# Kernel tuning notes

Hardware: AMD Instinct MI355X
Metric: run time of the kernel (lower is better)

Reference implementation:

```python
import jax, jax.numpy as jnp
import numpy as np

D_IN = 1024
D_OUT = 1024


def setup_inputs() -> dict:
    key = jax.random.key(0)
    kx, kq, kk, kv = jax.random.split(key, 4)
    B, T = 8, 2048
    x = jax.random.normal(kx, (B, T, D_IN), dtype=jnp.float32)
    # torch Linear weight is (d_out, d_in); we store transposed (d_in, d_out)
    s = 1.0 / np.sqrt(D_IN)
    Wq = jax.random.uniform(kq, (D_IN, D_OUT), jnp.float32, -s, s)
    Wk = jax.random.uniform(kk, (D_IN, D_OUT), jnp.float32, -s, s)
    Wv = jax.random.uniform(kv, (D_IN, D_OUT), jnp.float32, -s, s)
    return {"x": x, "Wq": Wq, "Wk": Wk, "Wv": Wv}


def reference(x, Wq, Wk, Wv):
    # x: (B, T, d_in)
    T = x.shape[1]
    d_out = Wq.shape[1]
    q = jnp.einsum('btd,de->bte', x, Wq)  # (B,T,d_out)
    k = jnp.einsum('btd,de->bte', x, Wk)
    v = jnp.einsum('btd,de->bte', x, Wv)
    scores = jnp.einsum('bqe,bke->bqk', q, k)  # (B,T,T)
    causal = jnp.tril(jnp.ones((T, T), dtype=bool))  # True = keep
    scores = jnp.where(causal[None], scores, -jnp.inf)
    weights = jax.nn.softmax(scores / jnp.sqrt(jnp.asarray(d_out, x.dtype)), axis=-1)
    # dropout p=0.0 -> identity
    return jnp.einsum('bqk,bke->bqe', weights, v)  # (B,T,d_out)
```

## Files before the change

### kernel.cpp

```cpp
#include <hip/hip_runtime.h>

using u16 = unsigned short;
typedef __bf16 bf16x8 __attribute__((ext_vector_type(8)));
typedef unsigned short u16x8 __attribute__((ext_vector_type(8)));
typedef float floatx4 __attribute__((ext_vector_type(4)));

__device__ __forceinline__ u16 f2bf(float f) {
  union { float f; unsigned u; } c; c.f = f;
  unsigned u = c.u;
  u += 0x7fffu + ((u >> 16) & 1u);
  return (u16)(u >> 16);
}
__device__ __forceinline__ float bf2f(u16 h) {
  union { unsigned u; float f; } c; c.u = ((unsigned)h) << 16; return c.f;
}

__device__ __forceinline__ void st_out(float* p, float v) { *p = v; }
__device__ __forceinline__ void st_out(u16* p, float v) { *p = f2bf(v); }

__device__ __forceinline__ void load16(const u16* g, u16* l) {
  __builtin_amdgcn_global_load_lds(
      (const __attribute__((address_space(1))) void*)g,
      (__attribute__((address_space(3))) void*)l, 16, 0, 0);
}

#define TILE 128
#define BK 64

template<typename OutT>
__device__ __forceinline__ void gemm_core(
    const u16* __restrict__ A, int lda, long sA,
    const u16* __restrict__ Bt, int ldb, long sB,
    OutT* __restrict__ C, int ldc, long sC,
    int kmax, int bx, int by, int bz, int tid)
{
  __shared__ u16 As[TILE * BK];
  __shared__ u16 Bs[TILE * BK];

  const u16* Ab = A + bz * sA + (long)by * TILE * lda;
  const u16* Bb = Bt + bz * sB + (long)bx * TILE * ldb;

  int lane = tid & 63;
  int wm = ((tid >> 7) & 1) * 64;
  int wn = ((tid >> 6) & 1) * 64;

  floatx4 acc[4][4] = {};
  int arow = wm + (lane & 15);
  int brow = wn + (lane & 15);
  int q = lane >> 4;

  for (int k0 = 0; k0 < kmax; k0 += BK) {
    __syncthreads();
#pragma unroll
    for (int h = 0; h < 4; h++) {
      int cc = tid + h * 256;
      int row = cc >> 3, gm = (cc & 7) ^ (row & 7);
      load16(Ab + (long)row * lda + k0 + gm * 8, &As[cc * 8]);
    }
#pragma unroll
    for (int h = 0; h < 4; h++) {
      int cc = tid + h * 256;
      int row = cc >> 3, gm = (cc & 7) ^ (row & 7);
      load16(Bb + (long)row * ldb + k0 + gm * 8, &Bs[cc * 8]);
    }
    __builtin_amdgcn_s_waitcnt(0);
    __syncthreads();

#pragma unroll
    for (int kp = 0; kp < 2; kp++) {
      bf16x8 a[4], b[4];
#pragma unroll
      for (int i = 0; i < 4; i++) {
        int r = arow + i * 16;
        a[i] = *(const bf16x8*)&As[(r * 8 + ((kp * 4 + q) ^ (r & 7))) * 8];
      }
#pragma unroll
      for (int j = 0; j < 4; j++) {
        int r = brow + j * 16;
        b[j] = *(const bf16x8*)&Bs[(r * 8 + ((kp * 4 + q) ^ (r & 7))) * 8];
      }
#pragma unroll
      for (int i = 0; i < 4; i++)
#pragma unroll
        for (int j = 0; j < 4; j++)
          acc[i][j] = __builtin_amdgcn_mfma_f32_16x16x32_bf16(a[i], b[j], acc[i][j], 0, 0, 0);
    }
  }

  OutT* Cb = C + bz * sC;
  int colbase = bx * TILE + wn + (lane & 15);
  int rowbase = by * TILE + wm + ((lane >> 4) << 2);
#pragma unroll
  for (int i = 0; i < 4; i++)
#pragma unroll
    for (int j = 0; j < 4; j++) {
      int col = colbase + j * 16;
#pragma unroll
      for (int r = 0; r < 4; r++)
        st_out(&Cb[(long)(rowbase + i * 16 + r) * ldc + col], acc[i][j][r]);
    }
}

template<typename OutT>
__global__ __launch_bounds__(256, 2)
void gemm_rect(const u16* __restrict__ A, int lda, long sA,
               const u16* __restrict__ Bt, int ldb, long sB,
               OutT* __restrict__ C, int ldc, long sC, int K,
               int l2gx, int nO8s)
{
  int L = blockIdx.x;
  int t = ((L & 7) << nO8s) | (L >> 3);
  int bx = t & ((1 << l2gx) - 1), by = t >> l2gx;
  gemm_core<OutT>(A, lda, sA, Bt, ldb, sB, C, ldc, sC, K, bx, by, blockIdx.y, threadIdx.x);
}

__global__ __launch_bounds__(256, 2)
void gemm_tri(const u16* __restrict__ A, int lda, long sA,
              const u16* __restrict__ Bt, int ldb, long sB,
              u16* __restrict__ C, int ldc, long sC, int K)
{
  int tp = blockIdx.x;
  int g = (tp & 7) * 17 + (tp >> 3);
  int sr = 0, sc = 0, pre = 0;
  for (;;) {
    int sz = (sr == sc) ? 3 : 4;
    if (pre + sz > g) break;
    pre += sz; ++sc;
    if (sc > sr) { ++sr; sc = 0; }
  }
  int w = g - pre;
  int r, c;
  if (sr == sc) { r = 2 * sr + (w > 0); c = 2 * sc + (w == 2); }
  else          { r = 2 * sr + (w >> 1); c = 2 * sc + (w & 1); }
  gemm_core<u16>(A, lda, sA, Bt, ldb, sB, C, ldc, sC, K, c, r, blockIdx.y, threadIdx.x);
}

__global__ __launch_bounds__(256, 2)
void gemm_opv(const u16* __restrict__ P, int lda, long sA,
              const u16* __restrict__ VT, int ldb, long sB,
              float* __restrict__ C, int ldc, long sC)
{
  int L = blockIdx.x;
  int j = L & 7, s = L >> 3;
  int by = (s < 8) ? 15 - j : j;
  int bx = s & 7;
  gemm_core<float>(P, lda, sA, VT, ldb, sB, C, ldc, sC,
                   (by + 1) * TILE, bx, by, blockIdx.y, threadIdx.x);
}

template<typename OutT>
__device__ __forceinline__ void gemm_core256(
    const u16* __restrict__ A, int lda, long sA,
    const u16* __restrict__ Bt, int ldb, long sB,
    OutT* __restrict__ C, int ldc, long sC,
    int kmax, int bx, int by, int bz, int tid, u16* lds)
{
  const u16* Ab = A + bz * sA + (long)by * 256 * lda;
  const u16* Bb = Bt + bz * sB + (long)bx * 256 * ldb;

  const int lane = tid & 63, wid = tid >> 6;
  const int wm = wid >> 2;
  const int wn = wid & 3;
  const int l15 = lane & 15, q = lane >> 4;

  const int cc0 = tid, cc1 = tid + 512;
  const int r0 = cc0 >> 3, g0 = (cc0 & 7) ^ (r0 & 7);
  const int r1 = cc1 >> 3, g1 = (cc1 & 7) ^ (r1 & 7);

  const int NK = kmax >> 6;

  floatx4 acc[8][4] = {};

  auto STAGE_A = [&](int k, int half, int buf) {
    const u16* g = Ab + (long)(half * 128) * lda + k * 64;
    load16(g + (long)r0 * lda + g0 * 8, lds + buf + half * 8192 + cc0 * 8);
    load16(g + (long)r1 * lda + g1 * 8, lds + buf + half * 8192 + cc1 * 8);
  };
  auto STAGE_B = [&](int k, int half, int buf) {
    const u16* g = Bb + (long)(half * 128) * ldb + k * 64;
    load16(g + (long)r0 * ldb + g0 * 8, lds + buf + 16384 + half * 8192 + cc0 * 8);
    load16(g + (long)r1 * ldb + g1 * 8, lds + buf + 16384 + half * 8192 + cc1 * 8);
  };

  STAGE_B(0, 0, 0); STAGE_B(0, 1, 0);
  STAGE_A(0, 0, 0); STAGE_A(0, 1, 0);
  if (NK > 1) {
    STAGE_B(1, 0, 32768); STAGE_B(1, 1, 32768);
    STAGE_A(1, 0, 32768);
    asm volatile("s_waitcnt vmcnt(6)" ::: "memory");
  } else {
    asm volatile("s_waitcnt vmcnt(0)" ::: "memory");
  }
  __builtin_amdgcn_s_barrier();

  const int s0 = (q ^ (l15 & 7)) * 8;
  const int s1 = ((q + 4) ^ (l15 & 7)) * 8;

  bf16x8 aL[2][4], aH[2][4], bL[2][2], bH[2][2];

  for (int t = 0; t < NK; ++t) {
    const int buf = (t & 1) ? 32768 : 0;
    const int nbuf = 32768 - buf;
    const int abase = buf + wm * 8192 + l15 * 64;
    const int bbase = buf + 16384 + (wn >> 1) * 8192 + ((wn & 1) * 64 + l15) * 64;

#pragma unroll
    for (int i = 0; i < 4; ++i) {
      aL[0][i] = *(const bf16x8*)&lds[abase + i * 1024 + s0];
      aL[1][i] = *(const bf16x8*)&lds[abase + i * 1024 + s1];
    }
#pragma unroll
    for (int j = 0; j < 2; ++j) {
      bL[0][j] = *(const bf16x8*)&lds[bbase + j * 1024 + s0];
      bL[1][j] = *(const bf16x8*)&lds[bbase + j * 1024 + s1];
    }
    if (t + 1 < NK) STAGE_A(t + 1, 1, nbuf);
    asm volatile("s_waitcnt lgkmcnt(8)" ::: "memory");
    __builtin_amdgcn_s_barrier();
    asm volatile("s_waitcnt lgkmcnt(0)" ::: "memory");
    __builtin_amdgcn_s_setprio(1);
#pragma unroll
    for (int kp = 0; kp < 2; ++kp)
#pragma unroll
      for (int i = 0; i < 4; ++i)
#pragma unroll
        for (int j = 0; j < 2; ++j)
          acc[i][j] = __builtin_amdgcn_mfma_f32_16x16x32_bf16(aL[kp][i], bL[kp][j], acc[i][j], 0, 0, 0);
    __builtin_amdgcn_s_setprio(0);
    asm volatile("" ::: "memory");
    __builtin_amdgcn_s_barrier();

#pragma unroll
    for (int j = 0; j < 2; ++j) {
      bH[0][j] = *(const bf16x8*)&lds[bbase + (2 + j) * 1024 + s0];
      bH[1][j] = *(const bf16x8*)&lds[bbase + (2 + j) * 1024 + s1];
    }
    asm volatile("" ::: "memory");
    __builtin_amdgcn_s_barrier();
    asm volatile("s_waitcnt lgkmcnt(0)" ::: "memory");
    __builtin_amdgcn_s_setprio(1);
#pragma unroll
    for (int kp = 0; kp < 2; ++kp)
#pragma unroll
      for (int i = 0; i < 4; ++i)
#pragma unroll
        for (int j = 0; j < 2; ++j)
          acc[i][2 + j] = __builtin_amdgcn_mfma_f32_16x16x32_bf16(aL[kp][i], bH[kp][j], acc[i][2 + j], 0, 0, 0);
    __builtin_amdgcn_s_setprio(0);
    asm volatile("" ::: "memory");
    __builtin_amdgcn_s_barrier();

#pragma unroll
    for (int i = 0; i < 4; ++i) {
      aH[0][i] = *(const bf16x8*)&lds[abase + 4096 + i * 1024 + s0];
      aH[1][i] = *(const bf16x8*)&lds[abase + 4096 + i * 1024 + s1];
    }
    if (t + 2 < NK) { STAGE_B(t + 2, 0, buf); STAGE_B(t + 2, 1, buf); }
    asm volatile("" ::: "memory");
    __builtin_amdgcn_s_barrier();
    asm volatile("s_waitcnt lgkmcnt(0)" ::: "memory");
    __builtin_amdgcn_s_setprio(1);
#pragma unroll
    for (int kp = 0; kp < 2; ++kp)
#pragma unroll
      for (int i = 0; i < 4; ++i)
#pragma unroll
        for (int j = 0; j < 2; ++j)
          acc[4 + i][2 + j] = __builtin_amdgcn_mfma_f32_16x16x32_bf16(aH[kp][i], bH[kp][j], acc[4 + i][2 + j], 0, 0, 0);
    __builtin_amdgcn_s_setprio(0);
    asm volatile("" ::: "memory");
    __builtin_amdgcn_s_barrier();

    if (t + 2 < NK) {
      STAGE_A(t + 2, 0, buf);
      asm volatile("s_waitcnt vmcnt(6)" ::: "memory");
    } else {
      asm volatile("s_waitcnt vmcnt(0)" ::: "memory");
    }
    __builtin_amdgcn_s_barrier();
    __builtin_amdgcn_s_setprio(1);
#pragma unroll
    for (int kp = 0; kp < 2; ++kp)
#pragma unroll
      for (int i = 0; i < 4; ++i)
#pragma unroll
        for (int j = 0; j < 2; ++j)
          acc[4 + i][j] = __builtin_amdgcn_mfma_f32_16x16x32_bf16(aH[kp][i], bL[kp][j], acc[4 + i][j], 0, 0, 0);
    __builtin_amdgcn_s_setprio(0);
    asm volatile("" ::: "memory");
    __builtin_amdgcn_s_barrier();
  }

  OutT* Cb = C + bz * sC;
  const int colbase = bx * 256 + wn * 64 + l15;
  const int rowbase = by * 256 + wm * 128 + (q << 2);
#pragma unroll
  for (int i = 0; i < 8; ++i)
#pragma unroll
    for (int j = 0; j < 4; ++j) {
      const int col = colbase + j * 16;
#pragma unroll
      for (int r = 0; r < 4; ++r)
        st_out(&Cb[(long)(rowbase + i * 16 + r) * ldc + col], acc[i][j][r]);
    }
}

__global__ __launch_bounds__(512, 2)
void gemm256_proj(const u16* __restrict__ xb, const u16* __restrict__ NT,
                  const u16* __restrict__ WvT, u16* __restrict__ Yb,
                  u16* __restrict__ VT)
{
  extern __shared__ u16 lds[];
  int L = blockIdx.x;
  int t = ((L & 7) << 6) | (L >> 3);
  bool h = (t >= 256);
  int tt = h ? (t - 256) : t;
  int bx = h ? (tt & 63) : (tt & 3);
  int by = h ? (tt >> 6) : (tt >> 2);
  gemm_core256<u16>(h ? WvT : xb, 1024, 0L,
                    h ? xb : NT, 1024, 0L,
                    h ? VT : Yb, h ? 16384 : 1024, 0L,
                    1024, bx, by, 0, (int)threadIdx.x, lds);
}

__global__ __launch_bounds__(256)
void cvt_x(const float4* __restrict__ x, u16* __restrict__ o, int n4, float scale)
{
  int i = blockIdx.x * 256 + threadIdx.x;
  if (i >= n4) return;
  float4 v = x[i];
  ushort4 r;
  r.x = f2bf(v.x * scale); r.y = f2bf(v.y * scale);
  r.z = f2bf(v.z * scale); r.w = f2bf(v.w * scale);
  *(ushort4*)(o + (long)i * 4) = r;
}

__global__ __launch_bounds__(256)
void cvt_qk(const float4* __restrict__ Wq, const float4* __restrict__ Wk,
            u16* __restrict__ oq, u16* __restrict__ ok, int n4)
{
  int i = blockIdx.x * 256 + threadIdx.x;
  if (i < n4) {
    float4 v = Wq[i];
    ushort4 r;
    r.x = f2bf(v.x * 0.03125f); r.y = f2bf(v.y * 0.03125f);
    r.z = f2bf(v.z * 0.03125f); r.w = f2bf(v.w * 0.03125f);
    *(ushort4*)(oq + (long)i * 4) = r;
  } else if (i < 2 * n4) {
    int k = i - n4;
    float4 v = Wk[k];
    ushort4 r;
    r.x = f2bf(v.x); r.y = f2bf(v.y); r.z = f2bf(v.z); r.w = f2bf(v.w);
    *(ushort4*)(ok + (long)k * 4) = r;
  }
}

__global__ __launch_bounds__(256)
void cvt_w(const float* __restrict__ W, u16* __restrict__ O)
{
  const int D = 1024;
  __shared__ float t[64][65];
  int tid = threadIdx.x;
  int c = tid & 63, r = tid >> 6;
  int e0 = blockIdx.x * 64, d0 = blockIdx.y * 64;
  for (int rr = r; rr < 64; rr += 4)
    t[rr][c] = W[(long)(d0 + rr) * D + e0 + c];
  __syncthreads();
  for (int rr = r; rr < 64; rr += 4)
    O[(long)(e0 + rr) * D + d0 + c] = f2bf(t[c][rr]);
}

__global__ __launch_bounds__(256)
void softmax_bf16(u16* __restrict__ S)
{
  const int T = 2048;
  int row = blockIdx.x & (T - 1);
  u16* Prow = S + (long)blockIdx.x * T;
  int n = row + 1;
  int W = ((row >> 7) + 1) << 7;
  int tid = threadIdx.x, lane = tid & 63, wid = tid >> 6;
  int i0 = tid * 8;
  bool act = (i0 < W);

  float v[8];
  float lmax = -3.0e38f;
  if (act) {
    u16x8 pv = *(const u16x8*)(Prow + i0);
#pragma unroll
    for (int j = 0; j < 8; j++) {
      v[j] = (i0 + j < n) ? bf2f(pv[j]) : -3.0e38f;
      lmax = fmaxf(lmax, v[j]);
    }
  }
  __shared__ float red[8];
#pragma unroll
  for (int o = 32; o > 0; o >>= 1) lmax = fmaxf(lmax, __shfl_down(lmax, o, 64));
  if (lane == 0) red[wid] = lmax;
  __syncthreads();
  float m = fmaxf(fmaxf(red[0], red[1]), fmaxf(red[2], red[3]));

  float lsum = 0.f;
  if (act) {
#pragma unroll
    for (int j = 0; j < 8; j++) {
      float e = (i0 + j < n) ? __expf(v[j] - m) : 0.f;
      v[j] = e;
      lsum += e;
    }
  }
#pragma unroll
  for (int o = 32; o > 0; o >>= 1) lsum += __shfl_down(lsum, o, 64);
  if (lane == 0) red[4 + wid] = lsum;
  __syncthreads();
  float inv = 1.0f / (red[4] + red[5] + red[6] + red[7]);

  if (act) {
    u16x8 w;
#pragma unroll
    for (int j = 0; j < 8; j++) w[j] = f2bf(v[j] * inv);
    *(u16x8*)(Prow + i0) = w;
  }
}

extern "C" void kernel_launch(void* const* d_in, const int* in_sizes, int n_in,
                              void* d_out, int out_size, void* d_ws, size_t ws_size,
                              hipStream_t stream)
{
  const int B = 8, T = 2048, D = 1024;
  const float* x  = (const float*)d_in[0];
  const float* Wq = (const float*)d_in[1];
  const float* Wk = (const float*)d_in[2];
  const float* Wv = (const float*)d_in[3];
  float* out = (float*)d_out;
  char* ws = (char*)d_ws;

  u16* xb  = (u16*)(ws);
  u16* WvT = (u16*)(ws + (32ul << 20));
  u16* NT  = (u16*)(ws + (34ul << 20));
  u16* Yb  = (u16*)(ws + (36ul << 20));
  u16* Wqb = Yb;
  u16* Wkb = (u16*)(ws + (38ul << 20));
  u16* VT  = (u16*)(ws + (68ul << 20));
  u16* S   = (u16*)(ws + (100ul << 20));

  const size_t OFF_S = 100ul << 20;
  int NB = 8;
  while (NB > 1 && OFF_S + (size_t)NB * T * T * 2 > ws_size) NB >>= 1;

  static bool attr_done = false;
  if (!attr_done) {
    hipFuncSetAttribute(reinterpret_cast<const void*>(gemm256_proj),
                        hipFuncAttributeMaxDynamicSharedMemorySize, 131072);
    attr_done = true;
  }

  cvt_x<<<(B * T * D / 4 + 255) / 256, 256, 0, stream>>>((const float4*)x, xb, B * T * D / 4, 1.0f);
  cvt_qk<<<(2 * D * D / 4 + 255) / 256, 256, 0, stream>>>(
      (const float4*)Wq, (const float4*)Wk, Wqb, Wkb, D * D / 4);
  cvt_w<<<dim3(16, 16), 256, 0, stream>>>(Wv, WvT);

  gemm_rect<u16><<<dim3(64, 1), 256, 0, stream>>>(
      Wkb, D, 0L, Wqb, D, 0L, NT, D, 0L, D, 3, 3);
  gemm256_proj<<<dim3(512, 1), 512, 131072, stream>>>(xb, NT, WvT, Yb, VT);

  for (int b0 = 0; b0 < B; b0 += NB) {
    gemm_tri<<<dim3(136, NB), 256, 0, stream>>>(
        Yb + (long)b0 * T * D, D, (long)T * D,
        xb + (long)b0 * T * D, D, (long)T * D,
        S, T, (long)T * T, D);
    softmax_bf16<<<NB * T, 256, 0, stream>>>(S);
    gemm_opv<<<dim3(128, NB), 256, 0, stream>>>(
        S, T, (long)T * T,
        VT + (long)b0 * T, B * T, (long)T,
        out + (long)b0 * T * D, D, (long)T * D);
  }
}
```

Baseline: 367.5 us.

## Fuse softmax normalization into the PV GEMM A-tile load using row stats

The softmax kernel that rewrote the bf16 score matrix is replaced by a row-statistics kernel that stores only each row's max and inverse sum. The P·V GEMM now gets its own inline mainloop. It loads raw scores through registers, applies exp, normalization and the causal mask, then writes the resulting P tile to LDS. This removes the full write-back of normalized probabilities. In exchange, the exponentials are recomputed for every output column tile, and the A operand no longer uses async global-to-LDS loads, which can stall the GEMM mainloop.

After: 402.1 us. 9.4% more time.

```diff
diff --git a/kernel.cpp b/kernel.cpp
--- a/kernel.cpp
+++ b/kernel.cpp
@@ -135,17 +135,151 @@
   gemm_core<u16>(A, lda, sA, Bt, ldb, sB, C, ldc, sC, K, c, r, blockIdx.y, threadIdx.x);
 }
 
+__global__ __launch_bounds__(256)
+void rowstat(const u16* __restrict__ S, float2* __restrict__ MI)
+{
+  const int T = 2048;
+  int row = blockIdx.x & (T - 1);
+  const u16* Prow = S + (long)blockIdx.x * T;
+  int n = row + 1;
+  int W = ((row >> 7) + 1) << 7;
+  int tid = threadIdx.x, lane = tid & 63, wid = tid >> 6;
+  int i0 = tid * 8;
+  bool act = (i0 < W);
+
+  float v[8];
+  float lmax = -3.0e38f;
+  if (act) {
+    u16x8 pv = *(const u16x8*)(Prow + i0);
+#pragma unroll
+    for (int j = 0; j < 8; j++) {
+      v[j] = (i0 + j < n) ? bf2f(pv[j]) : -3.0e38f;
+      lmax = fmaxf(lmax, v[j]);
+    }
+  }
+  __shared__ float red[8];
+#pragma unroll
+  for (int o = 32; o > 0; o >>= 1) lmax = fmaxf(lmax, __shfl_down(lmax, o, 64));
+  if (lane == 0) red[wid] = lmax;
+  __syncthreads();
+  float m = fmaxf(fmaxf(red[0], red[1]), fmaxf(red[2], red[3]));
+
+  float lsum = 0.f;
+  if (act) {
+#pragma unroll
+    for (int j = 0; j < 8; j++)
+      lsum += (i0 + j < n) ? __expf(v[j] - m) : 0.f;
+  }
+#pragma unroll
+  for (int o = 32; o > 0; o >>= 1) lsum += __shfl_down(lsum, o, 64);
+  if (lane == 0) red[4 + wid] = lsum;
+  __syncthreads();
+  if (tid == 0) {
+    float2 mi;
+    mi.x = m;
+    mi.y = 1.0f / (red[4] + red[5] + red[6] + red[7]);
+    MI[blockIdx.x] = mi;
+  }
+}
+
 __global__ __launch_bounds__(256, 2)
 void gemm_opv(const u16* __restrict__ P, int lda, long sA,
               const u16* __restrict__ VT, int ldb, long sB,
-              float* __restrict__ C, int ldc, long sC)
+              float* __restrict__ C, int ldc, long sC,
+              const float2* __restrict__ MI)
 {
   int L = blockIdx.x;
-  int j = L & 7, s = L >> 3;
-  int by = (s < 8) ? 15 - j : j;
+  int jj0 = L & 7, s = L >> 3;
+  int by = (s < 8) ? 15 - jj0 : jj0;
   int bx = s & 7;
-  gemm_core<float>(P, lda, sA, VT, ldb, sB, C, ldc, sC,
-                   (by + 1) * TILE, bx, by, blockIdx.y, threadIdx.x);
+  int bz = blockIdx.y;
+  int kmax = (by + 1) * TILE;
+
+  __shared__ u16 As[TILE * BK];
+  __shared__ u16 Bs[TILE * BK];
+
+  const u16* Ab = P + bz * sA + (long)by * TILE * lda;
+  const u16* Bb = VT + bz * sB + (long)bx * TILE * ldb;
+  int tid = threadIdx.x;
+
+  int lane = tid & 63;
+  int wm = ((tid >> 7) & 1) * 64;
+  int wn = ((tid >> 6) & 1) * 64;
+
+  floatx4 acc[4][4] = {};
+  int arow = wm + (lane & 15);
+  int brow = wn + (lane & 15);
+  int q = lane >> 4;
+
+  float mr[4], iv[4];
+  int qr[4];
+#pragma unroll
+  for (int h = 0; h < 4; h++) {
+    int cc = tid + h * 256;
+    int row = cc >> 3;
+    qr[h] = by * TILE + row;
+    float2 mi = MI[bz * 2048 + qr[h]];
+    mr[h] = mi.x; iv[h] = mi.y;
+  }
+
+  for (int k0 = 0; k0 < kmax; k0 += BK) {
+    __syncthreads();
+#pragma unroll
+    for (int h = 0; h < 4; h++) {
+      int cc = tid + h * 256;
+      int row = cc >> 3, gm = (cc & 7) ^ (row & 7);
+      load16(Bb + (long)row * ldb + k0 + gm * 8, &Bs[cc * 8]);
+    }
+#pragma unroll
+    for (int h = 0; h < 4; h++) {
+      int cc = tid + h * 256;
+      int row = cc >> 3, gm = (cc & 7) ^ (row & 7);
+      int c0 = k0 + gm * 8;
+      u16x8 raw = *(const u16x8*)(Ab + (long)row * lda + c0);
+      u16x8 ov;
+#pragma unroll
+      for (int j = 0; j < 8; j++) {
+        float p = (c0 + j <= qr[h]) ? __expf(bf2f(raw[j]) - mr[h]) * iv[h] : 0.f;
+        ov[j] = f2bf(p);
+      }
+      *(u16x8*)&As[cc * 8] = ov;
+    }
+    __builtin_amdgcn_s_waitcnt(0);
+    __syncthreads();
+
+#pragma unroll
+    for (int kp = 0; kp < 2; kp++) {
+      bf16x8 a[4], b[4];
+#pragma unroll
+      for (int i = 0; i < 4; i++) {
+        int r = arow + i * 16;
+        a[i] = *(const bf16x8*)&As[(r * 8 + ((kp * 4 + q) ^ (r & 7))) * 8];
+      }
+#pragma unroll
+      for (int j = 0; j < 4; j++) {
+        int r = brow + j * 16;
+        b[j] = *(const bf16x8*)&Bs[(r * 8 + ((kp * 4 + q) ^ (r & 7))) * 8];
+      }
+#pragma unroll
+      for (int i = 0; i < 4; i++)
+#pragma unroll
+        for (int j = 0; j < 4; j++)
+          acc[i][j] = __builtin_amdgcn_mfma_f32_16x16x32_bf16(a[i], b[j], acc[i][j], 0, 0, 0);
+    }
+  }
+
+  float* Cb = C + bz * sC;
+  int colbase = bx * TILE + wn + (lane & 15);
+  int rowbase = by * TILE + wm + ((lane >> 4) << 2);
+#pragma unroll
+  for (int i = 0; i < 4; i++)
+#pragma unroll
+    for (int j = 0; j < 4; j++) {
+      int col = colbase + j * 16;
+#pragma unroll
+      for (int r = 0; r < 4; r++)
+        Cb[(long)(rowbase + i * 16 + r) * ldc + col] = acc[i][j][r];
+    }
 }
 
 template<typename OutT>
@@ -370,58 +504,6 @@
     O[(long)(e0 + rr) * D + d0 + c] = f2bf(t[c][rr]);
 }
 
-__global__ __launch_bounds__(256)
-void softmax_bf16(u16* __restrict__ S)
-{
-  const int T = 2048;
-  int row = blockIdx.x & (T - 1);
-  u16* Prow = S + (long)blockIdx.x * T;
-  int n = row + 1;
-  int W = ((row >> 7) + 1) << 7;
-  int tid = threadIdx.x, lane = tid & 63, wid = tid >> 6;
-  int i0 = tid * 8;
-  bool act = (i0 < W);
-
-  float v[8];
-  float lmax = -3.0e38f;
-  if (act) {
-    u16x8 pv = *(const u16x8*)(Prow + i0);
-#pragma unroll
-    for (int j = 0; j < 8; j++) {
-      v[j] = (i0 + j < n) ? bf2f(pv[j]) : -3.0e38f;
-      lmax = fmaxf(lmax, v[j]);
-    }
-  }
-  __shared__ float red[8];
-#pragma unroll
-  for (int o = 32; o > 0; o >>= 1) lmax = fmaxf(lmax, __shfl_down(lmax, o, 64));
-  if (lane == 0) red[wid] = lmax;
-  __syncthreads();
-  float m = fmaxf(fmaxf(red[0], red[1]), fmaxf(red[2], red[3]));
-
-  float lsum = 0.f;
-  if (act) {
-#pragma unroll
-    for (int j = 0; j < 8; j++) {
-      float e = (i0 + j < n) ? __expf(v[j] - m) : 0.f;
-      v[j] = e;
-      lsum += e;
-    }
-  }
-#pragma unroll
-  for (int o = 32; o > 0; o >>= 1) lsum += __shfl_down(lsum, o, 64);
-  if (lane == 0) red[4 + wid] = lsum;
-  __syncthreads();
-  float inv = 1.0f / (red[4] + red[5] + red[6] + red[7]);
-
-  if (act) {
-    u16x8 w;
-#pragma unroll
-    for (int j = 0; j < 8; j++) w[j] = f2bf(v[j] * inv);
-    *(u16x8*)(Prow + i0) = w;
-  }
-}
-
 extern "C" void kernel_launch(void* const* d_in, const int* in_sizes, int n_in,
                               void* d_out, int out_size, void* d_ws, size_t ws_size,
                               hipStream_t stream)
@@ -442,6 +524,7 @@
   u16* Wkb = (u16*)(ws + (38ul << 20));
   u16* VT  = (u16*)(ws + (68ul << 20));
   u16* S   = (u16*)(ws + (100ul << 20));
+  float2* MI = (float2*)(ws + (34ul << 20));
 
   const size_t OFF_S = 100ul << 20;
   int NB = 8;
@@ -468,10 +551,11 @@
         Yb + (long)b0 * T * D, D, (long)T * D,
         xb + (long)b0 * T * D, D, (long)T * D,
         S, T, (long)T * T, D);
-    softmax_bf16<<<NB * T, 256, 0, stream>>>(S);
+    rowstat<<<NB * T, 256, 0, stream>>>(S, MI);
     gemm_opv<<<dim3(128, NB), 256, 0, stream>>>(
         S, T, (long)T * T,
         VT + (long)b0 * T, B * T, (long)T,
-        out + (long)b0 * T * D, D, (long)T * D);
-  }
-}
+        out + (long)b0 * T * D, D, (long)T * D,
+        MI);
+  }
+}
```

## Use wider 128x256 GEMM tiles for causal score and PV kernels

Applied to the files above, without the earlier changes.

Adds a gemm_core_w variant that computes 128x256 output tiles per block (each wave 128x64, 32 accumulators) and switches both the triangular QK^T score kernel and the P·V kernel to it. Block indexing is remapped accordingly, with a new triangular enumeration for the score tiles and half as many blocks per batch. The wider tiles raise arithmetic intensity and reuse of A tiles. In exchange they increase register pressure (128 accumulator floats per lane) and LDS usage, and causal tiles at the diagonal become coarser, so some masked work is wasted and fewer blocks are available for occupancy.

After: 371.8 us. No clear change (+1.2%).

```diff
diff --git a/kernel.cpp b/kernel.cpp
--- a/kernel.cpp
+++ b/kernel.cpp
@@ -114,25 +114,88 @@
   gemm_core<OutT>(A, lda, sA, Bt, ldb, sB, C, ldc, sC, K, bx, by, blockIdx.y, threadIdx.x);
 }
 
+template<typename OutT>
+__device__ __forceinline__ void gemm_core_w(
+    const u16* __restrict__ A, int lda, long sA,
+    const u16* __restrict__ Bt, int ldb, long sB,
+    OutT* __restrict__ C, int ldc, long sC,
+    int kmax, int bx, int by, int bz, int tid)
+{
+  __shared__ u16 As[128 * BK];
+  __shared__ u16 Bs[256 * BK];
+
+  const u16* Ab = A + bz * sA + (long)by * 128 * lda;
+  const u16* Bb = Bt + bz * sB + (long)bx * 256 * ldb;
+
+  int lane = tid & 63;
+  int wid = tid >> 6;
+  int l15 = lane & 15, q = lane >> 4;
+
+  floatx4 acc[8][4] = {};
+
+  for (int k0 = 0; k0 < kmax; k0 += BK) {
+    __syncthreads();
+#pragma unroll
+    for (int h = 0; h < 4; h++) {
+      int cc = tid + h * 256;
+      int row = cc >> 3, gm = (cc & 7) ^ (row & 7);
+      load16(Ab + (long)row * lda + k0 + gm * 8, &As[cc * 8]);
+    }
+#pragma unroll
+    for (int h = 0; h < 8; h++) {
+      int cc = tid + h * 256;
+      int row = cc >> 3, gm = (cc & 7) ^ (row & 7);
+      load16(Bb + (long)row * ldb + k0 + gm * 8, &Bs[cc * 8]);
+    }
+    __builtin_amdgcn_s_waitcnt(0);
+    __syncthreads();
+
+#pragma unroll
+    for (int kp = 0; kp < 2; kp++) {
+      bf16x8 a[8], b[4];
+#pragma unroll
+      for (int i = 0; i < 8; i++) {
+        int r = l15 + i * 16;
+        a[i] = *(const bf16x8*)&As[(r * 8 + ((kp * 4 + q) ^ (r & 7))) * 8];
+      }
+#pragma unroll
+      for (int j = 0; j < 4; j++) {
+        int r = wid * 64 + l15 + j * 16;
+        b[j] = *(const bf16x8*)&Bs[(r * 8 + ((kp * 4 + q) ^ (r & 7))) * 8];
+      }
+#pragma unroll
+      for (int i = 0; i < 8; i++)
+#pragma unroll
+        for (int j = 0; j < 4; j++)
+          acc[i][j] = __builtin_amdgcn_mfma_f32_16x16x32_bf16(a[i], b[j], acc[i][j], 0, 0, 0);
+    }
+  }
+
+  OutT* Cb = C + bz * sC;
+  int colbase = bx * 256 + wid * 64 + l15;
+  int rowbase = by * 128 + (q << 2);
+#pragma unroll
+  for (int i = 0; i < 8; i++)
+#pragma unroll
+    for (int j = 0; j < 4; j++) {
+      int col = colbase + j * 16;
+#pragma unroll
+      for (int r = 0; r < 4; r++)
+        st_out(&Cb[(long)(rowbase + i * 16 + r) * ldc + col], acc[i][j][r]);
+    }
+}
+
 __global__ __launch_bounds__(256, 2)
 void gemm_tri(const u16* __restrict__ A, int lda, long sA,
               const u16* __restrict__ Bt, int ldb, long sB,
               u16* __restrict__ C, int ldc, long sC, int K)
 {
   int tp = blockIdx.x;
-  int g = (tp & 7) * 17 + (tp >> 3);
-  int sr = 0, sc = 0, pre = 0;
-  for (;;) {
-    int sz = (sr == sc) ? 3 : 4;
-    if (pre + sz > g) break;
-    pre += sz; ++sc;
-    if (sc > sr) { ++sr; sc = 0; }
-  }
-  int w = g - pre;
-  int r, c;
-  if (sr == sc) { r = 2 * sr + (w > 0); c = 2 * sc + (w == 2); }
-  else          { r = 2 * sr + (w >> 1); c = 2 * sc + (w & 1); }
-  gemm_core<u16>(A, lda, sA, Bt, ldb, sB, C, ldc, sC, K, c, r, blockIdx.y, threadIdx.x);
+  int t = (tp & 7) * 9 + (tp >> 3);
+  int r = 0, pre = 0;
+  while (pre + (r / 2 + 1) <= t) { pre += r / 2 + 1; ++r; }
+  int cp = t - pre;
+  gemm_core_w<u16>(A, lda, sA, Bt, ldb, sB, C, ldc, sC, K, cp, r, blockIdx.y, threadIdx.x);
 }
 
 __global__ __launch_bounds__(256, 2)
@@ -142,10 +205,10 @@
 {
   int L = blockIdx.x;
   int j = L & 7, s = L >> 3;
-  int by = (s < 8) ? 15 - j : j;
-  int bx = s & 7;
-  gemm_core<float>(P, lda, sA, VT, ldb, sB, C, ldc, sC,
-                   (by + 1) * TILE, bx, by, blockIdx.y, threadIdx.x);
+  int by = (s < 4) ? 15 - j : j;
+  int bxp = s & 3;
+  gemm_core_w<float>(P, lda, sA, VT, ldb, sB, C, ldc, sC,
+                     (by + 1) * TILE, bxp, by, blockIdx.y, threadIdx.x);
 }
 
 template<typename OutT>
@@ -464,12 +527,12 @@
   gemm256_proj<<<dim3(512, 1), 512, 131072, stream>>>(xb, NT, WvT, Yb, VT);
 
   for (int b0 = 0; b0 < B; b0 += NB) {
-    gemm_tri<<<dim3(136, NB), 256, 0, stream>>>(
+    gemm_tri<<<dim3(72, NB), 256, 0, stream>>>(
         Yb + (long)b0 * T * D, D, (long)T * D,
         xb + (long)b0 * T * D, D, (long)T * D,
         S, T, (long)T * T, D);
     softmax_bf16<<<NB * T, 256, 0, stream>>>(S);
-    gemm_opv<<<dim3(128, NB), 256, 0, stream>>>(
+    gemm_opv<<<dim3(64, NB), 256, 0, stream>>>(
         S, T, (long)T * T,
         VT + (long)b0 * T, B * T, (long)T,
         out + (long)b0 * T * D, D, (long)T * D);
```
